# Performance work log

Measured on AMD Instinct MI355X. Metric: run time of the kernel, lower is better.

## Reference

```python
import jax, jax.numpy as jnp
import numpy as np

B, LSEQ = 128, 4096
NUM_EXPERTS, TOP_K = 8, 2
OUT_SEQ = 256
AUX_FACTOR = 0.01


def _conv1d(x, w, b, stride, pad):
    # x: [B, Cin, L], w: [Cout, Cin, K]
    y = jax.lax.conv_general_dilated(x, w, (stride,), [(pad, pad)],
                                     dimension_numbers=('NCH', 'OIH', 'NCH'))
    return y + b[None, :, None]


def setup_inputs() -> dict:
    key = jax.random.key(0)
    ks = jax.random.split(key, 9)
    s = 0.05
    return {
        'x': jax.random.normal(ks[0], (B, LSEQ), jnp.float32),
        # gating conv net (in_channels=2 -> 32 -> 64, kernel 5, padding same)
        'g_w1': jax.random.normal(ks[1], (32, 2, 5), jnp.float32) * s,
        'g_b1': jnp.zeros((32,), jnp.float32),
        'g_w2': jax.random.normal(ks[2], (64, 32, 5), jnp.float32) * s,
        'g_b2': jnp.zeros((64,), jnp.float32),
        # gating MLP (64 -> 128 -> num_experts)
        'm_w1': jax.random.normal(ks[3], (128, 64), jnp.float32) * s,
        'm_b1': jnp.zeros((128,), jnp.float32),
        'm_w2': jax.random.normal(ks[4], (NUM_EXPERTS, 128), jnp.float32) * s,
        'm_b2': jnp.zeros((NUM_EXPERTS,), jnp.float32),
        # expert CNN stacks, stacked over experts (same shapes per expert)
        'ew1': jax.random.normal(ks[5], (NUM_EXPERTS, 64, 2, 7), jnp.float32) * s,
        'eb1': jnp.zeros((NUM_EXPERTS, 64), jnp.float32),
        'ew2': jax.random.normal(ks[6], (NUM_EXPERTS, 128, 64, 5), jnp.float32) * s,
        'eb2': jnp.zeros((NUM_EXPERTS, 128), jnp.float32),
        'ew3': jax.random.normal(ks[7], (NUM_EXPERTS, 128, 128, 3), jnp.float32) * s,
        'eb3': jnp.zeros((NUM_EXPERTS, 128), jnp.float32),
    }


def reference(x, g_w1, g_b1, g_w2, g_b2, m_w1, m_b1, m_w2, m_b2,
              ew1, eb1, ew2, eb2, ew3, eb3):
    b, lseq = x.shape
    # periodic Hann window (torch.hann_window default)
    win = 0.5 * (1.0 - jnp.cos(2.0 * jnp.pi * jnp.arange(lseq, dtype=x.dtype) / lseq))
    xf = jnp.fft.rfft(x * win, norm='ortho')
    fft = jnp.stack([xf.real, xf.imag], axis=1)  # [B, 2, Lf]

    # gating: conv -> relu -> conv -> relu -> global avg pool -> MLP (dropout in eval)
    h = jax.nn.relu(_conv1d(fft, g_w1, g_b1, 1, 2))
    h = jax.nn.relu(_conv1d(h, g_w2, g_b2, 1, 2))
    pooled = h.mean(-1)  # [B, 64]
    logits = jax.nn.relu(pooled @ m_w1.T + m_b1) @ m_w2.T + m_b2  # [B, E]
    rw = jax.nn.softmax(logits, axis=1)
    aux = AUX_FACTOR * NUM_EXPERTS * (rw.mean(0) * logits.mean(0)).sum()

    tw, ti = jax.lax.top_k(rw, TOP_K)  # [B, K]
    tw = tw / tw.sum(-1, keepdims=True)

    # Each (token, k) pair routes fft[b] to expert ti[b,k]; compute each expert
    # densely over the batch and gather (same math as masked dispatch/combine).
    def expert(w1, b1, w2, b2, w3, b3):
        e = jax.nn.relu(_conv1d(fft, w1, b1, 2, 3))
        e = jax.nn.relu(_conv1d(e, w2, b2, 2, 2))
        e = jax.nn.relu(_conv1d(e, w3, b3, 1, 1))
        return e

    out_stack = jax.vmap(expert)(ew1, eb1, ew2, eb2, ew3, eb3)  # [E, B, C, L]
    sel = out_stack[ti, jnp.arange(b)[:, None]]                 # [B, K, C, L]
    final = (sel * tw[:, :, None, None]).sum(1)                 # [B, C, L]

    # adaptive max pool 1d to OUT_SEQ (PyTorch window rule)
    L = final.shape[-1]
    starts = np.floor(np.arange(OUT_SEQ) * L / OUT_SEQ).astype(np.int32)
    ends = np.ceil((np.arange(OUT_SEQ) + 1) * L / OUT_SEQ).astype(np.int32)
    maxw = int((ends - starts).max())
    raw = starts[:, None] + np.arange(maxw)[None, :]
    valid = jnp.asarray(raw < ends[:, None])
    idx = np.minimum(raw, L - 1)
    g = final[..., idx]  # [B, C, OUT_SEQ, maxw]
    resized = jnp.max(jnp.where(valid, g, -jnp.inf), axis=-1)
    return (resized, aux)
```

## Files before the change

### kernel.cpp

```cpp
#include <hip/hip_runtime.h>

#define NFREQ 2049
#define L1LEN 1025
#define L1STRIDE 1026
#define L2LEN 513

typedef short v8s  __attribute__((ext_vector_type(8)));
typedef float v16f __attribute__((ext_vector_type(16)));
typedef unsigned short ushort_t;
typedef unsigned int uint_t;

#define OFF_FFT     0ull
#define OFF_TWID    524544ull
#define OFF_PTW     526592ull
#define OFF_WIN     530944ull
#define OFF_PART    535040ull
#define OFF_TW      1075712ull
#define OFF_TI      1075968ull
#define OFF_SRWLOG  1076224ull
#define OFF_W2HF    1076480ull
#define OFF_W2LF    1081600ull
#define OFF_W2F     1086720ull
#define OFF_W3F     1250560ull
#define OFF_A       1447168ull
#define OFF_E2U     9852160ull

#define E1U_K_STRIDE 8404992
#define E2U_K_STRIDE 8404992

__device__ __forceinline__ float relu_f(float x) { return fmaxf(x, 0.0f); }
__device__ __forceinline__ int   rfl_i(int v)   { return __builtin_amdgcn_readfirstlane(v); }
__device__ __forceinline__ float rfl_f(float v) { return __uint_as_float((unsigned)__builtin_amdgcn_readfirstlane((int)__float_as_uint(v))); }
__device__ __forceinline__ ushort_t f2bf(float x) {
    unsigned u = __float_as_uint(x);
    unsigned r = (u + 0x7FFFu + ((u >> 16) & 1u)) >> 16;
    return (ushort_t)r;
}
__device__ __forceinline__ float bf2f(ushort_t h) { return __uint_as_float(((unsigned)h) << 16); }

__global__ void init_kernel(float* SRWLOG, float* TWID, float* PTW, float* WIN,
                            ushort_t* W2HF, ushort_t* W2LF, ushort_t* W2F, ushort_t* W3F,
                            const float* g_w2, const float* ew2, const float* ew3) {
    const float PI = 3.14159265358979323846f;
    int tid = blockIdx.x * blockDim.x + threadIdx.x;
    int stride = gridDim.x * blockDim.x;
    for (int i = tid; i < 16; i += stride) SRWLOG[i] = 0.0f;
    for (int j = tid; j < 1024; j += stride) {
        float a = PI * (float)j / 1024.0f;
        TWID[2 * j] = cosf(a);
        TWID[2 * j + 1] = -sinf(a);
    }
    for (int k = tid; k < 2049; k += stride) {
        float a = PI * (float)k / 2048.0f;
        PTW[2 * k] = cosf(a);
        PTW[2 * k + 1] = sinf(a);
    }
    for (int n = tid; n < 4096; n += stride) {
        WIN[n] = 0.5f * (1.0f - cosf(2.0f * PI * (float)n / 4096.0f));
    }
    for (int i = tid; i < 10240; i += stride) {
        int j = i & 7;
        int lane = (i >> 3) & 63;
        int ks = (i >> 9) & 1;
        int tile = (i >> 10) & 1;
        int t = i >> 11;
        int o = tile * 32 + (lane & 31);
        int c = ks * 16 + (lane >> 5) * 8 + j;
        float w = g_w2[o * 160 + c * 5 + t];
        ushort_t h = f2bf(w);
        W2HF[i] = h;
        W2LF[i] = f2bf(w - bf2f(h));
    }
    for (int i = tid; i < 327680; i += stride) {
        int j = i & 7;
        int lane = (i >> 3) & 63;
        int ks = (i >> 9) & 3;
        int w = (i >> 11) & 3;
        int t = (i >> 13) % 5;
        int e = i / 40960;
        int o = w * 32 + (lane & 31);
        int c = ks * 16 + (lane >> 5) * 8 + j;
        W2F[i] = f2bf(ew2[((e * 128 + o) * 64 + c) * 5 + t]);
    }
    for (int i = tid; i < 393216; i += stride) {
        int j = i & 7;
        int lane = (i >> 3) & 63;
        int ks = (i >> 9) & 7;
        int w = (i >> 12) & 3;
        int t = (i >> 14) % 3;
        int e = i / 49152;
        int o = w * 32 + (lane & 31);
        int c = ks * 16 + (lane >> 5) * 8 + j;
        W3F[i] = f2bf(ew3[((e * 128 + o) * 128 + c) * 3 + t]);
    }
}

__global__ __launch_bounds__(1024) void fft_kernel(const float* __restrict__ x,
                                                   const float* __restrict__ TWID,
                                                   const float* __restrict__ PTW,
                                                   const float* __restrict__ WIN,
                                                   float* __restrict__ FFT) {
    __shared__ float re[2048];
    __shared__ float im[2048];
    int b = blockIdx.x, t = threadIdx.x;
    const float* xb = x + b * 4096;
    for (int i = t; i < 2048; i += 1024) {
        int j = (int)(__brev((unsigned)i) >> 21);
        re[i] = xb[2 * j] * WIN[2 * j];
        im[i] = xb[2 * j + 1] * WIN[2 * j + 1];
    }
    for (int s = 1; s <= 11; ++s) {
        __syncthreads();
        int half = 1 << (s - 1);
        int shift = 11 - s;
        int bf = t;
        {
            int grp = bf >> (s - 1);
            int pos = bf & (half - 1);
            int i1 = (grp << s) + pos;
            int i2 = i1 + half;
            int j = pos << shift;
            float wr = TWID[2 * j], wi = TWID[2 * j + 1];
            float ar = re[i2], ai = im[i2];
            float tr = wr * ar - wi * ai;
            float ti = wr * ai + wi * ar;
            float br = re[i1], bi = im[i1];
            re[i2] = br - tr; im[i2] = bi - ti;
            re[i1] = br + tr; im[i1] = bi + ti;
        }
    }
    __syncthreads();
    const float scale = 1.0f / 64.0f;
    for (int k = t; k <= 2048; k += 1024) {
        int k1 = k & 2047;
        int k2 = (2048 - k) & 2047;
        float zr = re[k1], zi = im[k1];
        float yr = re[k2], yi = im[k2];
        float Er = 0.5f * (zr + yr), Ei = 0.5f * (zi - yi);
        float Or = 0.5f * (zi + yi), Oi = 0.5f * (yr - zr);
        float c2 = PTW[2 * k], s3 = PTW[2 * k + 1];
        FFT[b * 4098 + k]        = (Er + c2 * Or + s3 * Oi) * scale;
        FFT[b * 4098 + 2049 + k] = (Ei + c2 * Oi - s3 * Or) * scale;
    }
}

__global__ __launch_bounds__(256) void g12_kernel(const float* __restrict__ FFT,
                                                  const float* __restrict__ g_w1, const float* __restrict__ g_b1,
                                                  const ushort_t* __restrict__ W2HF, const ushort_t* __restrict__ W2LF,
                                                  const float* __restrict__ g_b2,
                                                  float* __restrict__ PART) {
    __shared__ float fx[2][72];
    __shared__ float w1S[320];
    __shared__ float b1S[32];
    __shared__ __align__(16) char un[17408];
    ushort_t (*xh)[40] = (ushort_t (*)[40])un;
    ushort_t (*xl)[40] = (ushort_t (*)[40])(un + 5440);
    float (*red)[68]  = (float (*)[68])un;
    int b = blockIdx.y;
    int q0 = blockIdx.x * 64;
    int t = threadIdx.x;
    for (int i = t; i < 352; i += 256) {
        if (i < 320) w1S[i] = g_w1[i];
        else b1S[i - 320] = g_b1[i - 320];
    }
    {
        const float* fb = FFT + b * 4098;
        for (int i = t; i < 144; i += 256) {
            int ch = i / 72, u = i % 72;
            int P = q0 - 4 + u;
            fx[ch][u] = (P >= 0 && P < NFREQ) ? fb[ch * NFREQ + P] : 0.0f;
        }
    }
    __syncthreads();
    {
        int c = t & 31;
        float bias = b1S[c];
        float wr[10];
        #pragma unroll
        for (int j = 0; j < 10; ++j) wr[j] = w1S[c * 10 + j];
        for (int i = t; i < 544; i += 256) {
            int g4 = (i >> 5) << 2;
            float4 x00 = *(const float4*)&fx[0][g4];
            float4 x01 = *(const float4*)&fx[0][g4 + 4];
            float4 x10 = *(const float4*)&fx[1][g4];
            float4 x11 = *(const float4*)&fx[1][g4 + 4];
            float xa[8] = {x00.x, x00.y, x00.z, x00.w, x01.x, x01.y, x01.z, x01.w};
            float xb_[8] = {x10.x, x10.y, x10.z, x10.w, x11.x, x11.y, x11.z, x11.w};
            #pragma unroll
            for (int rr = 0; rr < 4; ++rr) {
                int row = g4 + rr;
                int pos = q0 - 2 + row;
                ushort_t h = 0, l = 0;
                if (pos >= 0 && pos < NFREQ) {
                    float a = bias;
                    #pragma unroll
                    for (int tt = 0; tt < 5; ++tt) a = fmaf(xa[rr + tt], wr[tt], a);
                    #pragma unroll
                    for (int tt = 0; tt < 5; ++tt) a = fmaf(xb_[rr + tt], wr[5 + tt], a);
                    a = relu_f(a);
                    h = f2bf(a);
                    l = f2bf(a - bf2f(h));
                }
                xh[row][c] = h;
                xl[row][c] = l;
            }
        }
    }
    __syncthreads();
    int lane = t & 63;
    int w = rfl_i(t >> 6);
    int tile = w & 1;
    int qh = w >> 1;
    int n = lane & 31;
    int kg = lane >> 5;
    v16f acc;
    #pragma unroll
    for (int i = 0; i < 16; ++i) acc[i] = 0.0f;
    #pragma unroll
    for (int t5 = 0; t5 < 5; ++t5) {
        int row = qh * 32 + n + t5;
        #pragma unroll
        for (int ks = 0; ks < 2; ++ks) {
            int c0 = ks * 16 + kg * 8;
            v8s Ah = *(const v8s*)(W2HF + (((t5 * 2 + tile) * 2 + ks) << 9) + lane * 8);
            v8s Al = *(const v8s*)(W2LF + (((t5 * 2 + tile) * 2 + ks) << 9) + lane * 8);
            v8s Bh = *(const v8s*)&xh[row][c0];
            v8s Bl = *(const v8s*)&xl[row][c0];
            acc = __builtin_amdgcn_mfma_f32_32x32x16_bf16(Ah, Bh, acc, 0, 0, 0);
            acc = __builtin_amdgcn_mfma_f32_32x32x16_bf16(Ah, Bl, acc, 0, 0, 0);
            acc = __builtin_amdgcn_mfma_f32_32x32x16_bf16(Al, Bh, acc, 0, 0, 0);
        }
    }
    __syncthreads();
    {
        int q = q0 + qh * 32 + n;
        bool valid = (q < NFREQ);
        #pragma unroll
        for (int r = 0; r < 16; ++r) {
            int m = (r & 3) + 8 * (r >> 2) + 4 * kg;
            int o = tile * 32 + m;
            red[o][qh * 32 + n] = valid ? relu_f(acc[r] + g_b2[o]) : 0.0f;
        }
    }
    __syncthreads();
    {
        int o = t >> 2;
        int qq = t & 3;
        float s = 0.0f;
        #pragma unroll
        for (int u = 0; u < 4; ++u) {
            float4 vv = *(const float4*)&red[o][qq * 16 + u * 4];
            s += vv.x + vv.y + vv.z + vv.w;
        }
        s += __shfl_xor(s, 1, 64);
        s += __shfl_xor(s, 2, 64);
        if (qq == 0) PART[(b * 64 + o) * 66 + blockIdx.x] = s;
    }
}

__global__ __launch_bounds__(128) void mlp_kernel(const float* __restrict__ PART,
                                                  const float* __restrict__ m_w1, const float* __restrict__ m_b1,
                                                  const float* __restrict__ m_w2, const float* __restrict__ m_b2,
                                                  float* TW, int* TI, float* SRWLOG) {
    __shared__ float pooledS[64];
    __shared__ float hid[128];
    __shared__ float lgS[8];
    __shared__ float rwS[8];
    int b = blockIdx.x, t = threadIdx.x;
    if (t < 64) {
        float s = 0.0f;
        const float* pp = PART + (b * 64 + t) * 66;
        for (int blk = 0; blk < 33; ++blk) s += pp[blk];
        pooledS[t] = s;
    }
    __syncthreads();
    const float inv = 1.0f / 2049.0f;
    {
        float h = m_b1[t];
        for (int c = 0; c < 64; ++c)
            h = fmaf(pooledS[c] * inv, m_w1[t * 64 + c], h);
        hid[t] = relu_f(h);
    }
    __syncthreads();
    if (t < 8) {
        float lg = m_b2[t];
        for (int j = 0; j < 128; ++j) lg = fmaf(hid[j], m_w2[t * 128 + j], lg);
        lgS[t] = lg;
    }
    __syncthreads();
    if (t == 0) {
        float mx = lgS[0];
        for (int e = 1; e < 8; ++e) mx = fmaxf(mx, lgS[e]);
        float s = 0.0f, ex[8];
        for (int e = 0; e < 8; ++e) { ex[e] = expf(lgS[e] - mx); s += ex[e]; }
        for (int e = 0; e < 8; ++e) rwS[e] = ex[e] / s;
        int i1 = 0;
        for (int e = 1; e < 8; ++e) if (rwS[e] > rwS[i1]) i1 = e;
        int i2 = (i1 == 0) ? 1 : 0;
        for (int e = 0; e < 8; ++e) if (e != i1 && rwS[e] > rwS[i2]) i2 = e;
        float t0 = rwS[i1], t1 = rwS[i2], sm = t0 + t1;
        TW[b * 2] = t0 / sm; TW[b * 2 + 1] = t1 / sm;
        TI[b * 2] = i1; TI[b * 2 + 1] = i2;
    }
    __syncthreads();
    if (t < 8) {
        atomicAdd(&SRWLOG[t], rwS[t]);
        atomicAdd(&SRWLOG[8 + t], lgS[t]);
    }
}

__global__ void aux_kernel(const float* SRWLOG, float* out_aux) {
    if (threadIdx.x == 0 && blockIdx.x == 0) {
        float a = 0.0f;
        for (int e = 0; e < 8; ++e)
            a += (SRWLOG[e] / 128.0f) * (SRWLOG[8 + e] / 128.0f);
        out_aux[0] = 0.01f * 8.0f * a;
    }
}

__global__ __launch_bounds__(256) void e1_kernel(const float* __restrict__ FFT,
                                                 const float* __restrict__ ew1, const float* __restrict__ eb1,
                                                 const int* __restrict__ TI, ushort_t* __restrict__ E1u) {
    __shared__ float xs[2][520];
    int r0 = blockIdx.x * 256;
    int b = blockIdx.y;
    int k = blockIdx.z;
    int t = threadIdx.x;
    int e = rfl_i(TI[b * 2 + k]);
    int lo = 2 * r0 - 3;
    const float* fb = FFT + b * 4098;
    for (int i = t; i < 2 * 520; i += 256) {
        int ch = i / 520, off = i % 520;
        int pos = lo + off;
        xs[ch][off] = (pos >= 0 && pos < NFREQ) ? fb[ch * NFREQ + pos] : 0.0f;
    }
    __syncthreads();
    int r = r0 + t;
    if (r >= L1LEN) return;
    float xv[14];
    #pragma unroll
    for (int ch = 0; ch < 2; ++ch)
        #pragma unroll
        for (int tt = 0; tt < 7; ++tt)
            xv[ch * 7 + tt] = xs[ch][2 * t + tt];
    const float* wb = ew1 + e * 64 * 14;
    const float* bb = eb1 + e * 64;
    ushort_t* outb = E1u + (size_t)k * E1U_K_STRIDE + (size_t)b * 64 * L1STRIDE + r;
    bool last = (r == L1LEN - 1);
    for (int o = 0; o < 64; ++o) {
        float a = bb[o];
        const float* w = wb + o * 14;
        #pragma unroll
        for (int j = 0; j < 14; ++j)
            a = fmaf(xv[j], w[j], a);
        outb[o * L1STRIDE] = f2bf(relu_f(a));
        if (last) outb[o * L1STRIDE + 1] = 0;
    }
}

__global__ __launch_bounds__(256) void e2_kernel(const ushort_t* __restrict__ E1u,
                                                 const ushort_t* __restrict__ W2F, const float* __restrict__ eb2,
                                                 const int* __restrict__ TI, ushort_t* __restrict__ E2u) {
    __shared__ __align__(16) char sm2[19008];
    ushort_t (*xe)[72] = (ushort_t (*)[72])sm2;
    ushort_t (*xo)[72] = (ushort_t (*)[72])(sm2 + 9504);
    ushort_t (*oT)[136] = (ushort_t (*)[136])sm2;
    int b = blockIdx.x;
    int k = blockIdx.z;
    int q0 = blockIdx.y * 64;
    int t = threadIdx.x;
    int e = rfl_i(TI[b * 2 + k]);
    const ushort_t* E1k = E1u + (size_t)k * E1U_K_STRIDE;
    for (int i = t; i < 64 * 66; i += 256) {
        int c = i / 66, j = i % 66;
        int p = 2 * q0 - 2 + 2 * j;
        uint_t v = 0;
        if (p >= 0 && p < L1LEN)
            v = *(const uint_t*)(E1k + (size_t)(b * 64 + c) * L1STRIDE + p);
        xe[j][c] = (ushort_t)(v & 0xFFFFu);
        xo[j][c] = (ushort_t)(v >> 16);
    }
    __syncthreads();
    int lane = t & 63;
    int w = rfl_i(t >> 6);
    int n = lane & 31;
    int kg = lane >> 5;
    v16f acc0, acc1;
    #pragma unroll
    for (int i = 0; i < 16; ++i) { acc0[i] = 0.0f; acc1[i] = 0.0f; }
    #pragma unroll
    for (int t5 = 0; t5 < 5; ++t5) {
        int roff = t5 >> 1;
        const ushort_t (*sel)[72] = (t5 & 1) ? xo : xe;
        const ushort_t* wfrag = W2F + ((((e * 5 + t5) * 4 + w) * 4) << 9) + lane * 8;
        #pragma unroll
        for (int ks = 0; ks < 4; ++ks) {
            int c0 = ks * 16 + kg * 8;
            v8s a = *(const v8s*)(wfrag + (ks << 9));
            v8s b0 = *(const v8s*)&sel[n + roff][c0];
            v8s b1 = *(const v8s*)&sel[n + 32 + roff][c0];
            acc0 = __builtin_amdgcn_mfma_f32_32x32x16_bf16(a, b0, acc0, 0, 0, 0);
            acc1 = __builtin_amdgcn_mfma_f32_32x32x16_bf16(a, b1, acc1, 0, 0, 0);
        }
    }
    __syncthreads();
    #pragma unroll
    for (int g = 0; g < 4; ++g) {
        int ob = w * 32 + 8 * g + 4 * kg;
        uint_t p00 = (uint_t)f2bf(relu_f(acc0[4 * g + 0] + eb2[e * 128 + ob + 0]))
                   | ((uint_t)f2bf(relu_f(acc0[4 * g + 1] + eb2[e * 128 + ob + 1])) << 16);
        uint_t p01 = (uint_t)f2bf(relu_f(acc0[4 * g + 2] + eb2[e * 128 + ob + 2]))
                   | ((uint_t)f2bf(relu_f(acc0[4 * g + 3] + eb2[e * 128 + ob + 3])) << 16);
        uint_t p10 = (uint_t)f2bf(relu_f(acc1[4 * g + 0] + eb2[e * 128 + ob + 0]))
                   | ((uint_t)f2bf(relu_f(acc1[4 * g + 1] + eb2[e * 128 + ob + 1])) << 16);
        uint_t p11 = (uint_t)f2bf(relu_f(acc1[4 * g + 2] + eb2[e * 128 + ob + 2]))
                   | ((uint_t)f2bf(relu_f(acc1[4 * g + 3] + eb2[e * 128 + ob + 3])) << 16);
        uint2 v0; v0.x = p00; v0.y = p01;
        uint2 v1; v1.x = p10; v1.y = p11;
        *(uint2*)&oT[n][ob]      = v0;
        *(uint2*)&oT[32 + n][ob] = v1;
    }
    __syncthreads();
    ushort_t* E2k = E2u + (size_t)k * E2U_K_STRIDE;
    for (int i = t; i < 64 * 16; i += 256) {
        int qq = i >> 4, c8 = (i & 15) * 8;
        int q = q0 + qq;
        if (q < L2LEN)
            *(uint4*)(E2k + ((size_t)b * L2LEN + q) * 128 + c8) = *(const uint4*)&oT[qq][c8];
    }
}

__global__ __launch_bounds__(512) void e3_kernel(const ushort_t* __restrict__ E2u,
                                                 const ushort_t* __restrict__ W3F, const float* __restrict__ eb3,
                                                 const int* __restrict__ TI, const float* __restrict__ TW,
                                                 float* __restrict__ FINAL) {
    __shared__ __align__(16) ushort_t xT[2][66][136];
    int b = blockIdx.x;
    int q0 = blockIdx.y * 64;
    int t = threadIdx.x;
    int lane = t & 63;
    int w = rfl_i(t >> 6);
    int ow = w & 3;
    int qh = w >> 2;
    int n = lane & 31;
    int kg = lane >> 5;
    for (int i = t; i < 2112; i += 512) {
        int k = (i >= 1056) ? 1 : 0;
        int r = i - k * 1056;
        int row = r >> 4, c8 = (r & 15) * 8;
        int pos = q0 - 1 + row;
        uint4 v; v.x = 0u; v.y = 0u; v.z = 0u; v.w = 0u;
        if (pos >= 0 && pos < L2LEN)
            v = *(const uint4*)(E2u + (size_t)k * E2U_K_STRIDE + ((size_t)b * L2LEN + pos) * 128 + c8);
        *(uint4*)&xT[k][row][c8] = v;
    }
    __syncthreads();
    float res[16];
    #pragma unroll
    for (int i = 0; i < 16; ++i) res[i] = 0.0f;
    #pragma unroll
    for (int k = 0; k < 2; ++k) {
        int e = rfl_i(TI[b * 2 + k]);
        float wk = rfl_f(TW[b * 2 + k]);
        v16f acc;
        #pragma unroll
        for (int i = 0; i < 16; ++i) acc[i] = 0.0f;
        #pragma unroll
        for (int t3 = 0; t3 < 3; ++t3) {
            const ushort_t* wfrag = W3F + ((((e * 3 + t3) * 4 + ow) * 8) << 9) + lane * 8;
            #pragma unroll
            for (int ks = 0; ks < 8; ++ks) {
                int c0 = ks * 16 + kg * 8;
                v8s a = *(const v8s*)(wfrag + (ks << 9));
                v8s bb = *(const v8s*)&xT[k][qh * 32 + n + t3][c0];
                acc = __builtin_amdgcn_mfma_f32_32x32x16_bf16(a, bb, acc, 0, 0, 0);
            }
        }
        #pragma unroll
        for (int r = 0; r < 16; ++r) {
            int m = (r & 3) + 8 * (r >> 2) + 4 * kg;
            float bias = eb3[e * 128 + ow * 32 + m];
            res[r] += relu_f(acc[r] + bias) * wk;
        }
    }
    int q = q0 + qh * 32 + n;
    if (q < L2LEN) {
        float* Fb = FINAL + (size_t)b * 128 * 513;
        #pragma unroll
        for (int r = 0; r < 16; ++r) {
            int m = (r & 3) + 8 * (r >> 2) + 4 * kg;
            Fb[(ow * 32 + m) * 513 + q] = res[r];
        }
    }
}

__global__ __launch_bounds__(256) void pool_kernel(const float* __restrict__ FINAL,
                                                   float* __restrict__ out) {
    int idx = blockIdx.x * 256 + threadIdx.x;
    int j = idx & 255;
    int row = idx >> 8;
    const float* f = FINAL + (size_t)row * 513;
    int s = (513 * j) >> 8;
    int e_ = (513 * (j + 1) + 255) >> 8;
    float m = f[s];
    for (int p = s + 1; p < e_; ++p) m = fmaxf(m, f[p]);
    out[idx] = m;
}

extern "C" void kernel_launch(void* const* d_in, const int* in_sizes, int n_in,
                              void* d_out, int out_size, void* d_ws, size_t ws_size,
                              hipStream_t stream) {
    const float* x    = (const float*)d_in[0];
    const float* g_w1 = (const float*)d_in[1];
    const float* g_b1 = (const float*)d_in[2];
    const float* g_w2 = (const float*)d_in[3];
    const float* g_b2 = (const float*)d_in[4];
    const float* m_w1 = (const float*)d_in[5];
    const float* m_b1 = (const float*)d_in[6];
    const float* m_w2 = (const float*)d_in[7];
    const float* m_b2 = (const float*)d_in[8];
    const float* ew1  = (const float*)d_in[9];
    const float* eb1  = (const float*)d_in[10];
    const float* ew2  = (const float*)d_in[11];
    const float* eb2  = (const float*)d_in[12];
    const float* ew3  = (const float*)d_in[13];
    const float* eb3  = (const float*)d_in[14];

    float* ws     = (float*)d_ws;
    float* FFT    = ws + OFF_FFT;
    float* TWID   = ws + OFF_TWID;
    float* PTW    = ws + OFF_PTW;
    float* WIN    = ws + OFF_WIN;
    float* PART   = ws + OFF_PART;
    float* TW     = ws + OFF_TW;
    int*   TI     = (int*)(ws + OFF_TI);
    float* SRWLOG = ws + OFF_SRWLOG;
    ushort_t* W2HF = (ushort_t*)(ws + OFF_W2HF);
    ushort_t* W2LF = (ushort_t*)(ws + OFF_W2LF);
    ushort_t* W2F  = (ushort_t*)(ws + OFF_W2F);
    ushort_t* W3F  = (ushort_t*)(ws + OFF_W3F);
    ushort_t* E1u = (ushort_t*)(ws + OFF_A);
    float* FINAL  = ws + OFF_A;
    ushort_t* E2u = (ushort_t*)(ws + OFF_E2U);
    float* out    = (float*)d_out;

    init_kernel<<<512, 256, 0, stream>>>(SRWLOG, TWID, PTW, WIN, W2HF, W2LF, W2F, W3F, g_w2, ew2, ew3);
    fft_kernel<<<128, 1024, 0, stream>>>(x, TWID, PTW, WIN, FFT);
    g12_kernel<<<dim3(33, 128), 256, 0, stream>>>(FFT, g_w1, g_b1, W2HF, W2LF, g_b2, PART);
    mlp_kernel<<<128, 128, 0, stream>>>(PART, m_w1, m_b1, m_w2, m_b2, TW, TI, SRWLOG);
    aux_kernel<<<1, 64, 0, stream>>>(SRWLOG, out + 4194304);
    e1_kernel<<<dim3(5, 128, 2), 256, 0, stream>>>(FFT, ew1, eb1, TI, E1u);
    e2_kernel<<<dim3(128, 9, 2), 256, 0, stream>>>(E1u, W2F, eb2, TI, E2u);
    e3_kernel<<<dim3(128, 9), 512, 0, stream>>>(E2u, W3F, eb3, TI, TW, FINAL);
    pool_kernel<<<16384, 256, 0, stream>>>(FINAL, out);
}
```

Before: 234.8 us.

## Restructure e3 to reuse weight fragments across two tiles and prefetch second expert input

The e3 kernel now runs 256 threads where each wave computes both 32-row output tiles, so each loaded weight fragment feeds two MFMAs instead of one. The second expert's input rows are loaded into registers while the first expert's MFMAs run, then written to shared memory afterwards. The single-thread aux kernel is folded into pool_kernel to save one launch. The trade-offs are fewer waves per block and more register pressure from two accumulators plus the staged prefetch data.

```diff
diff --git a/kernel.cpp b/kernel.cpp
--- a/kernel.cpp
+++ b/kernel.cpp
@@ -309,15 +309,6 @@
     }
 }
 
-__global__ void aux_kernel(const float* SRWLOG, float* out_aux) {
-    if (threadIdx.x == 0 && blockIdx.x == 0) {
-        float a = 0.0f;
-        for (int e = 0; e < 8; ++e)
-            a += (SRWLOG[e] / 128.0f) * (SRWLOG[8 + e] / 128.0f);
-        out_aux[0] = 0.01f * 8.0f * a;
-    }
-}
-
 __global__ __launch_bounds__(256) void e1_kernel(const float* __restrict__ FFT,
                                                  const float* __restrict__ ew1, const float* __restrict__ eb1,
                                                  const int* __restrict__ TI, ushort_t* __restrict__ E1u) {
@@ -430,7 +421,7 @@
     }
 }
 
-__global__ __launch_bounds__(512) void e3_kernel(const ushort_t* __restrict__ E2u,
+__global__ __launch_bounds__(256) void e3_kernel(const ushort_t* __restrict__ E2u,
                                                  const ushort_t* __restrict__ W3F, const float* __restrict__ eb3,
                                                  const int* __restrict__ TI, const float* __restrict__ TW,
                                                  float* __restrict__ FINAL) {
@@ -439,63 +430,118 @@
     int q0 = blockIdx.y * 64;
     int t = threadIdx.x;
     int lane = t & 63;
-    int w = rfl_i(t >> 6);
-    int ow = w & 3;
-    int qh = w >> 2;
+    int ow = rfl_i(t >> 6);
     int n = lane & 31;
     int kg = lane >> 5;
-    for (int i = t; i < 2112; i += 512) {
-        int k = (i >= 1056) ? 1 : 0;
-        int r = i - k * 1056;
-        int row = r >> 4, c8 = (r & 15) * 8;
+    int e0  = rfl_i(TI[b * 2]);
+    int e1_ = rfl_i(TI[b * 2 + 1]);
+    float wk0 = rfl_f(TW[b * 2]);
+    float wk1 = rfl_f(TW[b * 2 + 1]);
+    for (int i = t; i < 1056; i += 256) {
+        int row = i >> 4, c8 = (i & 15) * 8;
         int pos = q0 - 1 + row;
         uint4 v; v.x = 0u; v.y = 0u; v.z = 0u; v.w = 0u;
         if (pos >= 0 && pos < L2LEN)
-            v = *(const uint4*)(E2u + (size_t)k * E2U_K_STRIDE + ((size_t)b * L2LEN + pos) * 128 + c8);
-        *(uint4*)&xT[k][row][c8] = v;
-    }
-    __syncthreads();
-    float res[16];
-    #pragma unroll
-    for (int i = 0; i < 16; ++i) res[i] = 0.0f;
-    #pragma unroll
-    for (int k = 0; k < 2; ++k) {
-        int e = rfl_i(TI[b * 2 + k]);
-        float wk = rfl_f(TW[b * 2 + k]);
-        v16f acc;
-        #pragma unroll
-        for (int i = 0; i < 16; ++i) acc[i] = 0.0f;
+            v = *(const uint4*)(E2u + ((size_t)b * L2LEN + pos) * 128 + c8);
+        *(uint4*)&xT[0][row][c8] = v;
+    }
+    __syncthreads();
+    uint4 st[5];
+    #pragma unroll
+    for (int j = 0; j < 5; ++j) {
+        int i = t + j * 256;
+        uint4 v; v.x = 0u; v.y = 0u; v.z = 0u; v.w = 0u;
+        if (i < 1056) {
+            int row = i >> 4, c8 = (i & 15) * 8;
+            int pos = q0 - 1 + row;
+            if (pos >= 0 && pos < L2LEN)
+                v = *(const uint4*)(E2u + (size_t)E2U_K_STRIDE + ((size_t)b * L2LEN + pos) * 128 + c8);
+        }
+        st[j] = v;
+    }
+    float res0[16], res1[16];
+    #pragma unroll
+    for (int i = 0; i < 16; ++i) { res0[i] = 0.0f; res1[i] = 0.0f; }
+    {
+        v16f a0, a1;
+        #pragma unroll
+        for (int i = 0; i < 16; ++i) { a0[i] = 0.0f; a1[i] = 0.0f; }
         #pragma unroll
         for (int t3 = 0; t3 < 3; ++t3) {
-            const ushort_t* wfrag = W3F + ((((e * 3 + t3) * 4 + ow) * 8) << 9) + lane * 8;
+            const ushort_t* wfrag = W3F + ((((e0 * 3 + t3) * 4 + ow) * 8) << 9) + lane * 8;
             #pragma unroll
             for (int ks = 0; ks < 8; ++ks) {
                 int c0 = ks * 16 + kg * 8;
                 v8s a = *(const v8s*)(wfrag + (ks << 9));
-                v8s bb = *(const v8s*)&xT[k][qh * 32 + n + t3][c0];
-                acc = __builtin_amdgcn_mfma_f32_32x32x16_bf16(a, bb, acc, 0, 0, 0);
+                v8s b0 = *(const v8s*)&xT[0][n + t3][c0];
+                v8s b1 = *(const v8s*)&xT[0][32 + n + t3][c0];
+                a0 = __builtin_amdgcn_mfma_f32_32x32x16_bf16(a, b0, a0, 0, 0, 0);
+                a1 = __builtin_amdgcn_mfma_f32_32x32x16_bf16(a, b1, a1, 0, 0, 0);
             }
         }
         #pragma unroll
         for (int r = 0; r < 16; ++r) {
             int m = (r & 3) + 8 * (r >> 2) + 4 * kg;
-            float bias = eb3[e * 128 + ow * 32 + m];
-            res[r] += relu_f(acc[r] + bias) * wk;
-        }
-    }
-    int q = q0 + qh * 32 + n;
-    if (q < L2LEN) {
-        float* Fb = FINAL + (size_t)b * 128 * 513;
+            float bias = eb3[e0 * 128 + ow * 32 + m];
+            res0[r] += relu_f(a0[r] + bias) * wk0;
+            res1[r] += relu_f(a1[r] + bias) * wk0;
+        }
+    }
+    #pragma unroll
+    for (int j = 0; j < 5; ++j) {
+        int i = t + j * 256;
+        if (i < 1056) {
+            int row = i >> 4, c8 = (i & 15) * 8;
+            *(uint4*)&xT[1][row][c8] = st[j];
+        }
+    }
+    __syncthreads();
+    {
+        v16f a0, a1;
+        #pragma unroll
+        for (int i = 0; i < 16; ++i) { a0[i] = 0.0f; a1[i] = 0.0f; }
+        #pragma unroll
+        for (int t3 = 0; t3 < 3; ++t3) {
+            const ushort_t* wfrag = W3F + ((((e1_ * 3 + t3) * 4 + ow) * 8) << 9) + lane * 8;
+            #pragma unroll
+            for (int ks = 0; ks < 8; ++ks) {
+                int c0 = ks * 16 + kg * 8;
+                v8s a = *(const v8s*)(wfrag + (ks << 9));
+                v8s b0 = *(const v8s*)&xT[1][n + t3][c0];
+                v8s b1 = *(const v8s*)&xT[1][32 + n + t3][c0];
+                a0 = __builtin_amdgcn_mfma_f32_32x32x16_bf16(a, b0, a0, 0, 0, 0);
+                a1 = __builtin_amdgcn_mfma_f32_32x32x16_bf16(a, b1, a1, 0, 0, 0);
+            }
+        }
         #pragma unroll
         for (int r = 0; r < 16; ++r) {
             int m = (r & 3) + 8 * (r >> 2) + 4 * kg;
-            Fb[(ow * 32 + m) * 513 + q] = res[r];
-        }
+            float bias = eb3[e1_ * 128 + ow * 32 + m];
+            res0[r] += relu_f(a0[r] + bias) * wk1;
+            res1[r] += relu_f(a1[r] + bias) * wk1;
+        }
+    }
+    float* Fb = FINAL + (size_t)b * 128 * 513;
+    int qA = q0 + n;
+    int qB = q0 + 32 + n;
+    #pragma unroll
+    for (int r = 0; r < 16; ++r) {
+        int m = (r & 3) + 8 * (r >> 2) + 4 * kg;
+        int o = ow * 32 + m;
+        if (qA < L2LEN) Fb[o * 513 + qA] = res0[r];
+        if (qB < L2LEN) Fb[o * 513 + qB] = res1[r];
     }
 }
 
 __global__ __launch_bounds__(256) void pool_kernel(const float* __restrict__ FINAL,
+                                                   const float* __restrict__ SRWLOG,
                                                    float* __restrict__ out) {
+    if (blockIdx.x == 0 && threadIdx.x == 0) {
+        float a = 0.0f;
+        for (int e = 0; e < 8; ++e)
+            a += (SRWLOG[e] / 128.0f) * (SRWLOG[8 + e] / 128.0f);
+        out[4194304] = 0.01f * 8.0f * a;
+    }
     int idx = blockIdx.x * 256 + threadIdx.x;
     int j = idx & 255;
     int row = idx >> 8;
@@ -548,9 +594,8 @@
     fft_kernel<<<128, 1024, 0, stream>>>(x, TWID, PTW, WIN, FFT);
     g12_kernel<<<dim3(33, 128), 256, 0, stream>>>(FFT, g_w1, g_b1, W2HF, W2LF, g_b2, PART);
     mlp_kernel<<<128, 128, 0, stream>>>(PART, m_w1, m_b1, m_w2, m_b2, TW, TI, SRWLOG);
-    aux_kernel<<<1, 64, 0, stream>>>(SRWLOG, out + 4194304);
     e1_kernel<<<dim3(5, 128, 2), 256, 0, stream>>>(FFT, ew1, eb1, TI, E1u);
     e2_kernel<<<dim3(128, 9, 2), 256, 0, stream>>>(E1u, W2F, eb2, TI, E2u);
-    e3_kernel<<<dim3(128, 9), 512, 0, stream>>>(E2u, W3F, eb3, TI, TW, FINAL);
-    pool_kernel<<<16384, 256, 0, stream>>>(FINAL, out);
-}
+    e3_kernel<<<dim3(128, 9), 256, 0, stream>>>(E2u, W3F, eb3, TI, TW, FINAL);
+    pool_kernel<<<16384, 256, 0, stream>>>(FINAL, SRWLOG, out);
+}
```

New measurement: 234.4 us. Within noise of the previous version (-0.2%).

## Fuse expert conv2 and conv3 into one kernel and fold aux into pool

Applied to the files above, without the earlier changes.

Merges the e2 and e3 kernels so the conv2 output tile, including a halo of 66 rows, is computed in shared memory and consumed directly by conv3, with no round trip through the global E2u buffer. Each block now handles both routed experts in sequence. It recomputes two halo rows per tile and uses fewer blocks, since the expert dimension is no longer a grid axis. The aux-loss scalar is moved into the pool kernel, which removes one launch.

```diff
diff --git a/kernel.cpp b/kernel.cpp
--- a/kernel.cpp
+++ b/kernel.cpp
@@ -26,7 +26,6 @@
 #define OFF_E2U     9852160ull
 
 #define E1U_K_STRIDE 8404992
-#define E2U_K_STRIDE 8404992
 
 __device__ __forceinline__ float relu_f(float x) { return fmaxf(x, 0.0f); }
 __device__ __forceinline__ int   rfl_i(int v)   { return __builtin_amdgcn_readfirstlane(v); }
@@ -309,15 +308,6 @@
     }
 }
 
-__global__ void aux_kernel(const float* SRWLOG, float* out_aux) {
-    if (threadIdx.x == 0 && blockIdx.x == 0) {
-        float a = 0.0f;
-        for (int e = 0; e < 8; ++e)
-            a += (SRWLOG[e] / 128.0f) * (SRWLOG[8 + e] / 128.0f);
-        out_aux[0] = 0.01f * 8.0f * a;
-    }
-}
-
 __global__ __launch_bounds__(256) void e1_kernel(const float* __restrict__ FFT,
                                                  const float* __restrict__ ew1, const float* __restrict__ eb1,
                                                  const int* __restrict__ TI, ushort_t* __restrict__ E1u) {
@@ -358,144 +348,126 @@
     }
 }
 
-__global__ __launch_bounds__(256) void e2_kernel(const ushort_t* __restrict__ E1u,
-                                                 const ushort_t* __restrict__ W2F, const float* __restrict__ eb2,
-                                                 const int* __restrict__ TI, ushort_t* __restrict__ E2u) {
-    __shared__ __align__(16) char sm2[19008];
-    ushort_t (*xe)[72] = (ushort_t (*)[72])sm2;
-    ushort_t (*xo)[72] = (ushort_t (*)[72])(sm2 + 9504);
-    ushort_t (*oT)[136] = (ushort_t (*)[136])sm2;
-    int b = blockIdx.x;
-    int k = blockIdx.z;
-    int q0 = blockIdx.y * 64;
-    int t = threadIdx.x;
-    int e = rfl_i(TI[b * 2 + k]);
-    const ushort_t* E1k = E1u + (size_t)k * E1U_K_STRIDE;
-    for (int i = t; i < 64 * 66; i += 256) {
-        int c = i / 66, j = i % 66;
-        int p = 2 * q0 - 2 + 2 * j;
-        uint_t v = 0;
-        if (p >= 0 && p < L1LEN)
-            v = *(const uint_t*)(E1k + (size_t)(b * 64 + c) * L1STRIDE + p);
-        xe[j][c] = (ushort_t)(v & 0xFFFFu);
-        xo[j][c] = (ushort_t)(v >> 16);
-    }
-    __syncthreads();
-    int lane = t & 63;
-    int w = rfl_i(t >> 6);
-    int n = lane & 31;
-    int kg = lane >> 5;
-    v16f acc0, acc1;
-    #pragma unroll
-    for (int i = 0; i < 16; ++i) { acc0[i] = 0.0f; acc1[i] = 0.0f; }
-    #pragma unroll
-    for (int t5 = 0; t5 < 5; ++t5) {
-        int roff = t5 >> 1;
-        const ushort_t (*sel)[72] = (t5 & 1) ? xo : xe;
-        const ushort_t* wfrag = W2F + ((((e * 5 + t5) * 4 + w) * 4) << 9) + lane * 8;
-        #pragma unroll
-        for (int ks = 0; ks < 4; ++ks) {
-            int c0 = ks * 16 + kg * 8;
-            v8s a = *(const v8s*)(wfrag + (ks << 9));
-            v8s b0 = *(const v8s*)&sel[n + roff][c0];
-            v8s b1 = *(const v8s*)&sel[n + 32 + roff][c0];
-            acc0 = __builtin_amdgcn_mfma_f32_32x32x16_bf16(a, b0, acc0, 0, 0, 0);
-            acc1 = __builtin_amdgcn_mfma_f32_32x32x16_bf16(a, b1, acc1, 0, 0, 0);
-        }
-    }
-    __syncthreads();
-    #pragma unroll
-    for (int g = 0; g < 4; ++g) {
-        int ob = w * 32 + 8 * g + 4 * kg;
-        uint_t p00 = (uint_t)f2bf(relu_f(acc0[4 * g + 0] + eb2[e * 128 + ob + 0]))
-                   | ((uint_t)f2bf(relu_f(acc0[4 * g + 1] + eb2[e * 128 + ob + 1])) << 16);
-        uint_t p01 = (uint_t)f2bf(relu_f(acc0[4 * g + 2] + eb2[e * 128 + ob + 2]))
-                   | ((uint_t)f2bf(relu_f(acc0[4 * g + 3] + eb2[e * 128 + ob + 3])) << 16);
-        uint_t p10 = (uint_t)f2bf(relu_f(acc1[4 * g + 0] + eb2[e * 128 + ob + 0]))
-                   | ((uint_t)f2bf(relu_f(acc1[4 * g + 1] + eb2[e * 128 + ob + 1])) << 16);
-        uint_t p11 = (uint_t)f2bf(relu_f(acc1[4 * g + 2] + eb2[e * 128 + ob + 2]))
-                   | ((uint_t)f2bf(relu_f(acc1[4 * g + 3] + eb2[e * 128 + ob + 3])) << 16);
-        uint2 v0; v0.x = p00; v0.y = p01;
-        uint2 v1; v1.x = p10; v1.y = p11;
-        *(uint2*)&oT[n][ob]      = v0;
-        *(uint2*)&oT[32 + n][ob] = v1;
-    }
-    __syncthreads();
-    ushort_t* E2k = E2u + (size_t)k * E2U_K_STRIDE;
-    for (int i = t; i < 64 * 16; i += 256) {
-        int qq = i >> 4, c8 = (i & 15) * 8;
-        int q = q0 + qq;
-        if (q < L2LEN)
-            *(uint4*)(E2k + ((size_t)b * L2LEN + q) * 128 + c8) = *(const uint4*)&oT[qq][c8];
-    }
-}
-
-__global__ __launch_bounds__(512) void e3_kernel(const ushort_t* __restrict__ E2u,
-                                                 const ushort_t* __restrict__ W3F, const float* __restrict__ eb3,
-                                                 const int* __restrict__ TI, const float* __restrict__ TW,
-                                                 float* __restrict__ FINAL) {
-    __shared__ __align__(16) ushort_t xT[2][66][136];
+__global__ __launch_bounds__(512) void e23_kernel(const ushort_t* __restrict__ E1u,
+                                                  const ushort_t* __restrict__ W2F, const float* __restrict__ eb2,
+                                                  const ushort_t* __restrict__ W3F, const float* __restrict__ eb3,
+                                                  const int* __restrict__ TI, const float* __restrict__ TW,
+                                                  float* __restrict__ FINAL) {
+    __shared__ __align__(16) ushort_t xe[98][72];
+    __shared__ __align__(16) ushort_t xo[98][72];
+    __shared__ __align__(16) ushort_t xT[66][136];
     int b = blockIdx.x;
     int q0 = blockIdx.y * 64;
     int t = threadIdx.x;
     int lane = t & 63;
     int w = rfl_i(t >> 6);
-    int ow = w & 3;
-    int qh = w >> 2;
     int n = lane & 31;
     int kg = lane >> 5;
-    for (int i = t; i < 2112; i += 512) {
-        int k = (i >= 1056) ? 1 : 0;
-        int r = i - k * 1056;
-        int row = r >> 4, c8 = (r & 15) * 8;
-        int pos = q0 - 1 + row;
-        uint4 v; v.x = 0u; v.y = 0u; v.z = 0u; v.w = 0u;
-        if (pos >= 0 && pos < L2LEN)
-            v = *(const uint4*)(E2u + (size_t)k * E2U_K_STRIDE + ((size_t)b * L2LEN + pos) * 128 + c8);
-        *(uint4*)&xT[k][row][c8] = v;
-    }
-    __syncthreads();
+    int ow3 = w & 3;
+    int qh3 = w >> 2;
     float res[16];
     #pragma unroll
     for (int i = 0; i < 16; ++i) res[i] = 0.0f;
-    #pragma unroll
     for (int k = 0; k < 2; ++k) {
         int e = rfl_i(TI[b * 2 + k]);
         float wk = rfl_f(TW[b * 2 + k]);
-        v16f acc;
-        #pragma unroll
-        for (int i = 0; i < 16; ++i) acc[i] = 0.0f;
-        #pragma unroll
-        for (int t3 = 0; t3 < 3; ++t3) {
-            const ushort_t* wfrag = W3F + ((((e * 3 + t3) * 4 + ow) * 8) << 9) + lane * 8;
+        const ushort_t* E1k = E1u + (size_t)k * E1U_K_STRIDE;
+        __syncthreads();
+        for (int i = t; i < 64 * 68; i += 512) {
+            int c = i / 68, j = i - c * 68;
+            int p = 2 * q0 - 4 + 2 * j;
+            uint_t v = 0;
+            if (p >= 0 && p < L1LEN)
+                v = *(const uint_t*)(E1k + (size_t)(b * 64 + c) * L1STRIDE + p);
+            xe[j][c] = (ushort_t)(v & 0xFFFFu);
+            xo[j][c] = (ushort_t)(v >> 16);
+        }
+        __syncthreads();
+        #pragma unroll
+        for (int rep = 0; rep < 2; ++rep) {
+            int tid = w + rep * 8;
+            if (tid < 12) {
+                int rt = tid >> 2, ot = tid & 3;
+                v16f acc;
+                #pragma unroll
+                for (int i = 0; i < 16; ++i) acc[i] = 0.0f;
+                #pragma unroll
+                for (int t5 = 0; t5 < 5; ++t5) {
+                    int roff = t5 >> 1;
+                    const ushort_t (*sel)[72] = (t5 & 1) ? xo : xe;
+                    const ushort_t* wfrag = W2F + ((((e * 5 + t5) * 4 + ot) * 4) << 9) + lane * 8;
+                    #pragma unroll
+                    for (int ks = 0; ks < 4; ++ks) {
+                        int c0 = ks * 16 + kg * 8;
+                        v8s a = *(const v8s*)(wfrag + (ks << 9));
+                        v8s bb = *(const v8s*)&sel[rt * 32 + n + roff][c0];
+                        acc = __builtin_amdgcn_mfma_f32_32x32x16_bf16(a, bb, acc, 0, 0, 0);
+                    }
+                }
+                int jj = rt * 32 + n;
+                if (jj < 66) {
+                    int qp = q0 - 1 + jj;
+                    bool ok = (qp >= 0 && qp < L2LEN);
+                    #pragma unroll
+                    for (int g = 0; g < 4; ++g) {
+                        int ob = ot * 32 + 8 * g + 4 * kg;
+                        uint_t p0 = 0, p1 = 0;
+                        if (ok) {
+                            p0 = (uint_t)f2bf(relu_f(acc[4 * g + 0] + eb2[e * 128 + ob + 0]))
+                               | ((uint_t)f2bf(relu_f(acc[4 * g + 1] + eb2[e * 128 + ob + 1])) << 16);
+                            p1 = (uint_t)f2bf(relu_f(acc[4 * g + 2] + eb2[e * 128 + ob + 2]))
+                               | ((uint_t)f2bf(relu_f(acc[4 * g + 3] + eb2[e * 128 + ob + 3])) << 16);
+                        }
+                        uint2 v; v.x = p0; v.y = p1;
+                        *(uint2*)&xT[jj][ob] = v;
+                    }
+                }
+            }
+        }
+        __syncthreads();
+        {
+            v16f a0;
             #pragma unroll
-            for (int ks = 0; ks < 8; ++ks) {
-                int c0 = ks * 16 + kg * 8;
-                v8s a = *(const v8s*)(wfrag + (ks << 9));
-                v8s bb = *(const v8s*)&xT[k][qh * 32 + n + t3][c0];
-                acc = __builtin_amdgcn_mfma_f32_32x32x16_bf16(a, bb, acc, 0, 0, 0);
+            for (int i = 0; i < 16; ++i) a0[i] = 0.0f;
+            #pragma unroll
+            for (int t3 = 0; t3 < 3; ++t3) {
+                const ushort_t* wfrag = W3F + ((((e * 3 + t3) * 4 + ow3) * 8) << 9) + lane * 8;
+                #pragma unroll
+                for (int ks = 0; ks < 8; ++ks) {
+                    int c0 = ks * 16 + kg * 8;
+                    v8s a = *(const v8s*)(wfrag + (ks << 9));
+                    v8s bb = *(const v8s*)&xT[qh3 * 32 + n + t3][c0];
+                    a0 = __builtin_amdgcn_mfma_f32_32x32x16_bf16(a, bb, a0, 0, 0, 0);
+                }
             }
-        }
+            #pragma unroll
+            for (int r = 0; r < 16; ++r) {
+                int m = (r & 3) + 8 * (r >> 2) + 4 * kg;
+                float bias = eb3[e * 128 + ow3 * 32 + m];
+                res[r] += relu_f(a0[r] + bias) * wk;
+            }
+        }
+    }
+    int q = q0 + qh3 * 32 + n;
+    if (q < L2LEN) {
+        float* Fb = FINAL + (size_t)b * 128 * 513;
         #pragma unroll
         for (int r = 0; r < 16; ++r) {
             int m = (r & 3) + 8 * (r >> 2) + 4 * kg;
-            float bias = eb3[e * 128 + ow * 32 + m];
-            res[r] += relu_f(acc[r] + bias) * wk;
-        }
-    }
-    int q = q0 + qh * 32 + n;
-    if (q < L2LEN) {
-        float* Fb = FINAL + (size_t)b * 128 * 513;
-        #pragma unroll
-        for (int r = 0; r < 16; ++r) {
-            int m = (r & 3) + 8 * (r >> 2) + 4 * kg;
-            Fb[(ow * 32 + m) * 513 + q] = res[r];
+            Fb[(ow3 * 32 + m) * 513 + q] = res[r];
         }
     }
 }
 
 __global__ __launch_bounds__(256) void pool_kernel(const float* __restrict__ FINAL,
+                                                   const float* __restrict__ SRWLOG,
                                                    float* __restrict__ out) {
+    if (blockIdx.x == 0 && threadIdx.x == 0) {
+        float a = 0.0f;
+        for (int e = 0; e < 8; ++e)
+            a += (SRWLOG[e] / 128.0f) * (SRWLOG[8 + e] / 128.0f);
+        out[4194304] = 0.01f * 8.0f * a;
+    }
     int idx = blockIdx.x * 256 + threadIdx.x;
     int j = idx & 255;
     int row = idx >> 8;
@@ -540,17 +512,14 @@
     ushort_t* W2F  = (ushort_t*)(ws + OFF_W2F);
     ushort_t* W3F  = (ushort_t*)(ws + OFF_W3F);
     ushort_t* E1u = (ushort_t*)(ws + OFF_A);
-    float* FINAL  = ws + OFF_A;
-    ushort_t* E2u = (ushort_t*)(ws + OFF_E2U);
+    float* FINAL  = ws + OFF_E2U;
     float* out    = (float*)d_out;
 
     init_kernel<<<512, 256, 0, stream>>>(SRWLOG, TWID, PTW, WIN, W2HF, W2LF, W2F, W3F, g_w2, ew2, ew3);
     fft_kernel<<<128, 1024, 0, stream>>>(x, TWID, PTW, WIN, FFT);
     g12_kernel<<<dim3(33, 128), 256, 0, stream>>>(FFT, g_w1, g_b1, W2HF, W2LF, g_b2, PART);
     mlp_kernel<<<128, 128, 0, stream>>>(PART, m_w1, m_b1, m_w2, m_b2, TW, TI, SRWLOG);
-    aux_kernel<<<1, 64, 0, stream>>>(SRWLOG, out + 4194304);
     e1_kernel<<<dim3(5, 128, 2), 256, 0, stream>>>(FFT, ew1, eb1, TI, E1u);
-    e2_kernel<<<dim3(128, 9, 2), 256, 0, stream>>>(E1u, W2F, eb2, TI, E2u);
-    e3_kernel<<<dim3(128, 9), 512, 0, stream>>>(E2u, W3F, eb3, TI, TW, FINAL);
-    pool_kernel<<<16384, 256, 0, stream>>>(FINAL, out);
-}
+    e23_kernel<<<dim3(128, 9), 512, 0, stream>>>(E1u, W2F, eb2, W3F, eb3, TI, TW, FINAL);
+    pool_kernel<<<16384, 256, 0, stream>>>(FINAL, SRWLOG, out);
+}
```

Result: slower. 243.8 us (+3.9%).
